# Kernel tuning notes

Measured on AMD Instinct MI355X. Metric: run time of the kernel, lower is better.

## Reference

```python
import jax, jax.numpy as jnp
import numpy as np

NC = 80          # num classes (len(yolov8.names))
CONF = 0.25      # ultralytics conf_thres default
IOU_T = 0.45     # ultralytics iou_thres default
MAX_DET = 300    # module default max_det
K = 1024         # pre-NMS candidate cap (static stand-in for max_nms)
MAX_WH = 7680.0  # ultralytics class-offset for multi-class NMS


def setup_inputs() -> dict:
    key = jax.random.key(0)
    k1, k2, k3 = jax.random.split(key, 3)
    B, A = 32, 8400
    # YOLOv8 head layout: rows 0:4 = xywh (pixels), rows 4: = sigmoid class scores
    xy = jax.random.uniform(k1, (B, 2, A), dtype=jnp.float32) * 640.0
    wh = jax.random.uniform(k2, (B, 2, A), dtype=jnp.float32) * 160.0 + 8.0
    scores = jax.random.uniform(k3, (B, NC, A), dtype=jnp.float32) ** 3  # mostly below conf_thres
    preds = jnp.concatenate([xy, wh, scores], axis=1)  # [B, 4+NC, A]
    return {"preds": preds}


def _box_iou(b):
    # b: [K, 4] xyxy -> [K, K] pairwise IoU
    area = (b[:, 2] - b[:, 0]) * (b[:, 3] - b[:, 1])
    lt = jnp.maximum(b[:, None, :2], b[None, :, :2])
    rb = jnp.minimum(b[:, None, 2:], b[None, :, 2:])
    wh = jnp.clip(rb - lt, 0.0)
    inter = wh[..., 0] * wh[..., 1]
    return inter / (area[:, None] + area[None, :] - inter + 1e-7)


def _nms_single(pred):
    # pred: [4+NC, A]
    boxes_xywh = pred[:4].T           # [A, 4]
    cls_scores = pred[4:].T           # [A, NC]
    conf = cls_scores.max(-1)         # best-class confidence per anchor
    cls = jnp.argmax(cls_scores, -1)
    score = jnp.where(conf > CONF, conf, 0.0)
    top, idx = jax.lax.top_k(score, K)            # K candidates by confidence
    xywh = boxes_xywh[idx]
    half = xywh[:, 2:] * 0.5
    boxes = jnp.concatenate([xywh[:, :2] - half, xywh[:, :2] + half], -1)  # xyxy
    cls_k = cls[idx]
    valid = top > CONF
    # multi-class NMS via per-class coordinate offset (ultralytics trick)
    iou = _box_iou(boxes + (cls_k.astype(boxes.dtype) * MAX_WH)[:, None])
    ar = jnp.arange(K)

    def body(i, st):
        supp, keep = st
        ki = valid[i] & ~supp[i]
        keep = keep.at[i].set(ki)
        supp = supp | (ki & (iou[i] > IOU_T) & (ar > i))
        return supp, keep

    _, keep = jax.lax.fori_loop(0, K, body,
                                (jnp.zeros(K, bool), jnp.zeros(K, bool)))
    fscore = jnp.where(keep, top, 0.0)
    sc, order = jax.lax.top_k(fscore, MAX_DET)
    det = jnp.concatenate(
        [boxes[order], top[order][:, None], cls_k[order].astype(boxes.dtype)[:, None]], -1)
    # pad invalid rows with value NC in every column (matches F.pad(value=len(names)))
    return jnp.where((sc > CONF)[:, None], det, jnp.float32(NC))


def reference(preds):
    # [B, MAX_DET, 6] -> (x1, y1, x2, y2, conf, cls), padded rows filled with NC
    return jax.vmap(_nms_single)(preds)
```

## Files before the change

### kernel.cpp

```cpp
#include <hip/hip_runtime.h>
#include <stdint.h>

typedef unsigned long long u64;
typedef unsigned int u32;

#define NC 80
#define CONF_T 0.25f
#define IOU_THR 0.45f
#define MAX_DET 300
#define KBIG 1024
#define A_ANCH 8400
#define NROWS 84
#define MAX_WH 7680.0f
#define HBINS 256
#define BIN_BASE 0x3e80u

__device__ __forceinline__ void hadd(u32* h, u32 bin, bool m, int lane) {
    u64 act = __ballot(m);
    if (act == 0) return;
    int fl = __ffsll((unsigned long long)act) - 1;
    u32 fb = __shfl(bin, fl);
    u64 same = __ballot(m && (bin == fb));
    if (lane == fl) atomicAdd(&h[fb], (u32)__popcll(same));
    if (m && (bin != fb)) atomicAdd(&h[bin], 1u);
}

__global__ __launch_bounds__(512) void yolo_conf_kernel(const float* __restrict__ preds,
                                                        u64* __restrict__ keys,
                                                        u32* __restrict__ hist) {
    int b = blockIdx.x / 9;
    int slab = blockIdx.x % 9;
    if (slab == 0 && threadIdx.x < HBINS) hist[(size_t)b * HBINS + threadIdx.x] = 0;
    int g = slab * 512 + threadIdx.x;
    if (g >= A_ANCH / 2) return;
    int a0 = g * 2;
    const float* base = preds + ((size_t)b * NROWS + 4) * A_ANCH + a0;
    float2 best = *(const float2*)base;
    int bc0 = 0, bc1 = 0;
#pragma unroll 8
    for (int c = 1; c < NC; ++c) {
        float2 v = *(const float2*)(base + (size_t)c * A_ANCH);
        if (v.x > best.x) { best.x = v.x; bc0 = c; }
        if (v.y > best.y) { best.y = v.y; bc1 = c; }
    }
    float s0 = (best.x > CONF_T) ? best.x : 0.0f;
    float s1 = (best.y > CONF_T) ? best.y : 0.0f;
    ulonglong2 kk;
    kk.x = ((u64)__float_as_uint(s0) << 32) | ((u64)(16383 - a0) << 7) | (u64)bc0;
    kk.y = ((u64)__float_as_uint(s1) << 32) | ((u64)(16383 - (a0 + 1)) << 7) | (u64)bc1;
    *(ulonglong2*)(keys + (size_t)b * A_ANCH + a0) = kk;
}

__global__ __launch_bounds__(256) void yolo_prep_kernel(const float* __restrict__ preds,
                                                        const u64* __restrict__ keys,
                                                        float4* __restrict__ obox,
                                                        u32* __restrict__ hist) {
    __shared__ u32 lh[HBINS];
    const int lane = threadIdx.x & 63;
    int b = blockIdx.x / 33;
    int a = (blockIdx.x % 33) * 256 + threadIdx.x;
    lh[threadIdx.x] = 0;
    __syncthreads();
    u32 bits = 0, bin = 0;
    bool act = a < A_ANCH;
    if (act) {
        u64 key = keys[(size_t)b * A_ANCH + a];
        bits = (u32)(key >> 32);
        int cls = (int)(key & 127u);
        const float* pb = preds + (size_t)b * NROWS * A_ANCH + a;
        float x = pb[0];
        float y = pb[A_ANCH];
        float w = pb[2 * A_ANCH];
        float h = pb[3 * A_ANCH];
        float hw = __fmul_rn(w, 0.5f), hh = __fmul_rn(h, 0.5f);
        float x1 = __fsub_rn(x, hw), x2 = __fadd_rn(x, hw);
        float y1 = __fsub_rn(y, hh), y2 = __fadd_rn(y, hh);
        float off = __fmul_rn((float)cls, MAX_WH);
        float4 oB;
        oB.x = __fadd_rn(x1, off); oB.y = __fadd_rn(y1, off);
        oB.z = __fadd_rn(x2, off); oB.w = __fadd_rn(y2, off);
        obox[(size_t)b * A_ANCH + a] = oB;
        bin = (bits >> 16) - BIN_BASE;
        if (bin > 255u) bin = 255u;
    }
    hadd(lh, bin, act && (bits != 0u), lane);
    __syncthreads();
    u32 c = lh[threadIdx.x];
    if (c) atomicAdd(&hist[(size_t)b * HBINS + threadIdx.x], c);
}

__device__ __forceinline__ float iou_f(float ix1, float iy1, float ix2, float iy2, float iar,
                                       float jx1, float jy1, float jx2, float jy2, float jar) {
    float lx = fmaxf(ix1, jx1), ly = fmaxf(iy1, jy1);
    float rx = fminf(ix2, jx2), ry = fminf(iy2, jy2);
    float ww = fmaxf(__fsub_rn(rx, lx), 0.0f);
    float hh = fmaxf(__fsub_rn(ry, ly), 0.0f);
    float inter = __fmul_rn(ww, hh);
    float den = __fadd_rn(__fsub_rn(__fadd_rn(iar, jar), inter), 1e-7f);
    return __fdiv_rn(inter, den);
}

__device__ __forceinline__ u64 bstep(u64 v, u32 idx, u32 size, u32 stride) {
    u64 v2 = __shfl_xor((unsigned long long)v, (int)stride, 64);
    bool keep_big = (((idx & stride) == 0) == ((idx & size) == 0));
    return ((v > v2) == keep_big) ? v : v2;
}

__device__ __forceinline__ void radix_scan(u32* hist, int nb, int shift, u32* s_scal,
                                           u32* wsum, int tid, int lane, int wid) {
    int per = nb >> 9; if (per == 0) per = 1;
    int na = nb / per;
    u32 rem = s_scal[1];
    u32 Pk = s_scal[0];
    int hi = nb - 1 - per * tid;
    u32 s = 0;
    if (tid < na)
        for (int q = 0; q < per; ++q) s += hist[hi - q];
    u32 pre = s;
#pragma unroll
    for (int off = 1; off < 64; off <<= 1) {
        u32 o = __shfl_up(pre, off);
        if (lane >= off) pre += o;
    }
    if (lane == 63) wsum[wid] = pre;
    __syncthreads();
    u32 base = 0;
    for (int w = 0; w < wid; ++w) base += wsum[w];
    u32 run = base + pre - s;
    if (tid < na) {
        for (int q = 0; q < per; ++q) {
            int d = hi - q;
            u32 g = hist[d];
            if (run < rem && rem <= run + g) {
                s_scal[0] = Pk | ((u32)d << shift);
                s_scal[1] = rem - run;
            }
            run += g;
        }
    }
    __syncthreads();
}

__global__ __launch_bounds__(512) void yolo_selsort_kernel(const u64* __restrict__ keys,
                                                           const u32* __restrict__ hist,
                                                           u64* __restrict__ sortk,
                                                           u32* __restrict__ meta) {
    const int b = blockIdx.x;
    const int tid = threadIdx.x;
    const int lane = tid & 63;
    const int wid = tid >> 6;

    __shared__ u64 skey[KBIG];
    __shared__ u32 wsum[8];
    __shared__ u32 s_scal[4];
    __shared__ u32 s_cnt;

    const u64* kb = keys + (size_t)b * A_ANCH;
    const u32* hb = hist + (size_t)b * HBINS;

    u32 hg = (tid < HBINS) ? hb[HBINS - 1 - tid] : 0u;
    u32 vals[17];
#pragma unroll
    for (int it = 0; it < 17; ++it) {
        int a = tid + it * 512;
        vals[it] = (a < A_ANCH) ? (u32)(kb[a] >> 32) : 0u;
    }
    {
        u32 pre = hg;
#pragma unroll
        for (int off = 1; off < 64; off <<= 1) {
            u32 o = __shfl_up(pre, off);
            if (lane >= off) pre += o;
        }
        if (lane == 63) wsum[wid] = pre;
        __syncthreads();
        u32 base = 0;
        for (int w = 0; w < wid; ++w) base += wsum[w];
        pre += base;
        u32 run = pre - hg;
        if (tid < HBINS) {
            if (run < 512u && 512u <= pre) { s_scal[0] = (u32)(HBINS - 1 - tid); s_scal[2] = pre; }
            if (tid == HBINS - 1) {
                s_scal[3] = pre;
                if (pre < 512u) { s_scal[0] = 0; s_scal[2] = pre; }
            }
        }
        __syncthreads();
    }
    const u32 Pbin16 = BIN_BASE + s_scal[0];
    const u32 Cfast = s_scal[2];
    const u32 validN = s_scal[3];
    if (tid == 0) { meta[b * 2] = Cfast; meta[b * 2 + 1] = validN; }
    if (Cfast > (u32)KBIG) return;

    skey[tid] = 0; skey[tid + 512] = 0;
    if (tid == 0) s_cnt = 0;
    __syncthreads();
#pragma unroll
    for (int it = 0; it < 17; ++it) {
        int a = tid + it * 512;
        u32 v = vals[it];
        bool take = (a < A_ANCH) && (v != 0u) && ((v >> 16) >= Pbin16);
        u64 m = __ballot(take);
        if (m) {
            int fl = __ffsll((unsigned long long)m) - 1;
            u32 basep = 0;
            if (lane == fl) basep = atomicAdd(&s_cnt, (u32)__popcll(m));
            basep = __shfl(basep, fl);
            if (take) {
                u32 pos = basep + (u32)__popcll(m & ((1ull << lane) - 1ull));
                if (pos < (u32)KBIG) skey[pos] = kb[a];
            }
        }
    }
    __syncthreads();

    {
        u64 vA = skey[tid], vB = skey[tid + 512];
        const u32 iA = (u32)tid, iB = (u32)tid + 512;
#pragma unroll
        for (u32 size = 2; size <= 64; size <<= 1)
#pragma unroll
            for (u32 stride = size >> 1; stride >= 1; stride >>= 1) {
                vA = bstep(vA, iA, size, stride);
                vB = bstep(vB, iB, size, stride);
            }
        skey[tid] = vA; skey[tid + 512] = vB;
        __syncthreads();
        for (u32 size = 128; size <= 1024; size <<= 1) {
            for (u32 stride = size >> 1; stride >= 64; stride >>= 1) {
                u32 i1 = ((tid & ~(int)(stride - 1)) << 1) | (tid & (stride - 1));
                u32 i2 = i1 + stride;
                bool desc = ((i1 & size) == 0);
                u64 x = skey[i1], y = skey[i2];
                if ((x < y) == desc) { skey[i1] = y; skey[i2] = x; }
                __syncthreads();
            }
            vA = skey[tid]; vB = skey[tid + 512];
#pragma unroll
            for (u32 stride = 32; stride >= 1; stride >>= 1) {
                vA = bstep(vA, iA, size, stride);
                vB = bstep(vB, iB, size, stride);
            }
            skey[tid] = vA; skey[tid + 512] = vB;
            __syncthreads();
        }
    }
    u64* so = sortk + (size_t)b * KBIG;
    so[tid] = skey[tid];
    so[tid + 512] = skey[tid + 512];
}

__global__ __launch_bounds__(512) void yolo_mat_kernel(const u64* __restrict__ sortk,
                                                       const float4* __restrict__ obox,
                                                       u64* __restrict__ rows) {
    const int b = blockIdx.x >> 3;
    const int m = blockIdx.x & 7;
    const int tid = threadIdx.x;
    const int lane = tid & 63;
    const int wid = tid >> 6;
    __shared__ float bx1[512], by1[512], bx2[512], by2[512], bar[512];

    const u64* sk = sortk + (size_t)b * KBIG;
    {
        u64 key = sk[tid];
        int idx = 16383 - (int)((key >> 7) & 16383u);
        if (idx >= A_ANCH || idx < 0) idx = 0;
        float4 ob = obox[(size_t)b * A_ANCH + idx];
        bx1[tid] = ob.x; by1[tid] = ob.y; bx2[tid] = ob.z; by2[tid] = ob.w;
        bar[tid] = __fmul_rn(__fsub_rn(ob.z, ob.x), __fsub_rn(ob.w, ob.y));
    }
    __syncthreads();

#pragma unroll
    for (int rr = 0; rr < 8; ++rr) {
        int i = m * 64 + wid * 8 + rr;
        float ix1 = bx1[i], iy1 = by1[i], ix2 = bx2[i], iy2 = by2[i], iar = bar[i];
        u64* rowp = rows + ((size_t)b * 512 + i) * 8;
#pragma unroll
        for (int wd = 0; wd < 8; ++wd) {
            int j = wd * 64 + lane;
            float iou = iou_f(ix1, iy1, ix2, iy2, iar, bx1[j], by1[j], bx2[j], by2[j], bar[j]);
            u64 mbit = __ballot((j > i) && (iou > IOU_THR));
            if (lane == 0) rowp[wd] = mbit;
        }
    }
}

union U2 {
    u32 hist[4096];
    struct { u32 eqw[264]; u32 wpre[264]; } tie;
};

__global__ __launch_bounds__(512) void yolo_recfb_kernel(const float* __restrict__ preds,
                                                         const u64* __restrict__ keys,
                                                         const u64* __restrict__ sortk,
                                                         const u64* __restrict__ rowsg,
                                                         const float4* __restrict__ obox,
                                                         const u32* __restrict__ hist,
                                                         const u32* __restrict__ meta,
                                                         float* __restrict__ out) {
    const int b = blockIdx.x;
    const int tid = threadIdx.x;
    const int lane = tid & 63;
    const int wid = tid >> 6;

    union SH {
        struct {
            u64 skl[512];
            u64 supp[8];
            u64 keep;
            int keptlist[364];
        } r;
        struct {
            U2 u2;
            u64 skey[KBIG];
            float BX1[KBIG], BY1[KBIG], BX2[KBIG], BY2[KBIG], BAR[KBIG];
            int keptlist[364];
            float kx1[364], ky1[364], kx2[364], ky2[364], kar[364];
            u32 kcls[364];
            u64 rows64[64];
        } f;
    };
    __shared__ SH sh;
    __shared__ u32 s_scal[4];
    __shared__ u32 wsum[8];
    __shared__ u32 s_cnt;
    __shared__ u32 s_csupp[2];
    __shared__ u32 s_nkept;

    const u32 Cfast0 = meta[b * 2];
    const u32 validN0 = meta[b * 2 + 1];

    sh.r.skl[tid] = sortk[(size_t)b * KBIG + tid];
    if (tid < 8) sh.r.supp[tid] = 0;
    if (tid == 0) s_nkept = 0;
    __syncthreads();

    bool ok = (Cfast0 <= (u32)KBIG);
    if (ok) {
        const u64* rb = rowsg + (size_t)b * 512 * 8;
        for (int c = 0; c < 8; ++c) {
            if (wid == 0) {
                int i = c * 64 + lane;
                u64 key = sh.r.skl[i];
                float sc = __uint_as_float((u32)(key >> 32));
                u64 ri = rb[(size_t)i * 8 + c];
                u64 validm = __ballot(sc > CONF_T) & ~sh.r.supp[c];
                u32 rlo = (u32)ri, rhi = (u32)(ri >> 32);
                u64 sup = 0, keep = 0;
#pragma unroll
                for (int i2 = 0; i2 < 64; ++i2) {
                    u64 rr = (((u64)(u32)__builtin_amdgcn_readlane((int)rhi, i2)) << 32) |
                             (u64)(u32)__builtin_amdgcn_readlane((int)rlo, i2);
                    bool ki = (((validm & ~sup) >> i2) & 1ull) != 0;
                    if (ki) { keep |= (1ull << i2); sup |= rr; }
                }
                u32 basek = s_nkept;
                if ((keep >> lane) & 1ull) {
                    u32 slot = basek + (u32)__popcll(keep & ((1ull << lane) - 1ull));
                    sh.r.keptlist[slot] = i;
                }
                if (lane == 0) { sh.r.keep = keep; s_nkept = basek + (u32)__popcll(keep); }
            }
            __syncthreads();
            {
                u64 k = sh.r.keep;
                u64 t = ((k >> lane) & 1ull) ? rb[(size_t)(c * 64 + lane) * 8 + wid] : 0ull;
#pragma unroll
                for (int off = 32; off >= 1; off >>= 1)
                    t |= (u64)__shfl_xor((unsigned long long)t, off, 64);
                if (lane == 0) sh.r.supp[wid] |= t;
            }
            __syncthreads();
            if (s_nkept >= MAX_DET) break;
        }
    }
    u32 nk0 = ok ? s_nkept : 0;
    bool fin = ok && ((nk0 >= MAX_DET) || (validN0 <= 512u));

    if (fin) {
        if (tid < MAX_DET) {
            float row[6];
            int t = (tid < (int)(nk0 < MAX_DET ? nk0 : MAX_DET)) ? sh.r.keptlist[tid] : -1;
            if (t >= 0) {
                u64 key = sh.r.skl[t];
                float score = __uint_as_float((u32)(key >> 32));
                int cls = (int)(key & 127u);
                int idx = 16383 - (int)((key >> 7) & 16383u);
                if (idx >= A_ANCH || idx < 0) idx = 0;
                const float* pb = preds + (size_t)b * NROWS * A_ANCH + idx;
                float x = pb[0], y = pb[A_ANCH], w = pb[2 * A_ANCH], h = pb[3 * A_ANCH];
                float hw = __fmul_rn(w, 0.5f), hh = __fmul_rn(h, 0.5f);
                row[0] = __fsub_rn(x, hw);
                row[1] = __fsub_rn(y, hh);
                row[2] = __fadd_rn(x, hw);
                row[3] = __fadd_rn(y, hh);
                row[4] = score;
                row[5] = (float)cls;
            } else {
                row[0] = row[1] = row[2] = row[3] = row[4] = row[5] = (float)NC;
            }
            float* o = out + ((size_t)b * MAX_DET + tid) * 6;
#pragma unroll
            for (int q = 0; q < 6; ++q) o[q] = row[q];
        }
        return;
    }

    __syncthreads();
    U2* u2 = &sh.f.u2;
    u64* skey = sh.f.skey;
    float* BX1 = sh.f.BX1; float* BY1 = sh.f.BY1;
    float* BX2 = sh.f.BX2; float* BY2 = sh.f.BY2; float* BAR = sh.f.BAR;
    int* keptlist = sh.f.keptlist;
    float* kx1 = sh.f.kx1; float* ky1 = sh.f.ky1;
    float* kx2 = sh.f.kx2; float* ky2 = sh.f.ky2; float* kar = sh.f.kar;
    u32* kcls = sh.f.kcls;
    u64* rows = sh.f.rows64;

    const u64* kb = keys + (size_t)b * A_ANCH;
    const u32* hb = hist + (size_t)b * HBINS;
    u32 hg = (tid < HBINS) ? hb[HBINS - 1 - tid] : 0u;
    u32 vals[17];
#pragma unroll
    for (int it = 0; it < 17; ++it) {
        int a = tid + it * 512;
        vals[it] = (a < A_ANCH) ? (u32)(kb[a] >> 32) : 0u;
    }
    {
        u32 pre = hg;
#pragma unroll
        for (int off = 1; off < 64; off <<= 1) {
            u32 o = __shfl_up(pre, off);
            if (lane >= off) pre += o;
        }
        if (lane == 63) wsum[wid] = pre;
        __syncthreads();
        u32 base = 0;
        for (int w = 0; w < wid; ++w) base += wsum[w];
        pre += base;
        u32 run = pre - hg;
        if (tid < HBINS) {
            if (run < 512u && 512u <= pre) { s_scal[0] = (u32)(HBINS - 1 - tid); s_scal[2] = pre; }
            if (tid == HBINS - 1) {
                s_scal[3] = pre;
                if (pre < 512u) { s_scal[0] = 0; s_scal[2] = pre; }
            }
        }
        __syncthreads();
    }
    const u32 Pbin16 = BIN_BASE + s_scal[0];
    const u32 Cfast = s_scal[2];
    const u32 validN = s_scal[3];

    for (int pass = 0; pass < 2; ++pass) {
        u32 Ccand;
        if (pass == 0) {
            if (Cfast > (u32)KBIG) continue;
            Ccand = Cfast;
            skey[tid] = 0; skey[tid + 512] = 0;
            if (tid == 0) { s_cnt = 0; s_nkept = 0; s_csupp[0] = 0; s_csupp[1] = 0; }
            __syncthreads();
#pragma unroll
            for (int it = 0; it < 17; ++it) {
                int a = tid + it * 512;
                u32 v = vals[it];
                bool take = (a < A_ANCH) && (v != 0u) && ((v >> 16) >= Pbin16);
                u64 m = __ballot(take);
                if (m) {
                    int fl = __ffsll((unsigned long long)m) - 1;
                    u32 basep = 0;
                    if (lane == fl) basep = atomicAdd(&s_cnt, (u32)__popcll(m));
                    basep = __shfl(basep, fl);
                    if (take) {
                        u32 pos = basep + (u32)__popcll(m & ((1ull << lane) - 1ull));
                        if (pos < (u32)KBIG) skey[pos] = kb[a];
                    }
                }
            }
            __syncthreads();
        } else {
            for (int i = tid; i < 4096; i += 512) u2->hist[i] = 0;
            if (tid == 0) {
                s_scal[0] = 0; s_scal[1] = (u32)KBIG; s_scal[2] = 0;
                s_nkept = 0; s_csupp[0] = 0; s_csupp[1] = 0;
            }
            __syncthreads();
#pragma unroll
            for (int it = 0; it < 17; ++it) {
                int a = tid + it * 512;
                hadd(u2->hist, vals[it] >> 20, a < A_ANCH, lane);
            }
            __syncthreads();
            radix_scan(u2->hist, 4096, 20, s_scal, wsum, tid, lane, wid);
            for (int i = tid; i < 4096; i += 512) u2->hist[i] = 0;
            __syncthreads();
            u32 Pk = s_scal[0];
#pragma unroll
            for (int it = 0; it < 17; ++it) {
                int a = tid + it * 512;
                u32 v = vals[it];
                bool m = (a < A_ANCH) && ((v & 0xFFF00000u) == Pk);
                hadd(u2->hist, (v >> 8) & 4095u, m, lane);
            }
            __syncthreads();
            radix_scan(u2->hist, 4096, 8, s_scal, wsum, tid, lane, wid);
            for (int i = tid; i < 256; i += 512) u2->hist[i] = 0;
            __syncthreads();
            Pk = s_scal[0];
#pragma unroll
            for (int it = 0; it < 17; ++it) {
                int a = tid + it * 512;
                u32 v = vals[it];
                bool m = (a < A_ANCH) && ((v & 0xFFFFFF00u) == Pk);
                hadd(u2->hist, v & 255u, m, lane);
            }
            __syncthreads();
            radix_scan(u2->hist, 256, 0, s_scal, wsum, tid, lane, wid);
            const u32 P = s_scal[0];
            const u32 tEq = s_scal[1];
            if (tid < 264) u2->tie.eqw[tid] = 0;
            __syncthreads();
#pragma unroll
            for (int it = 0; it < 17; ++it) {
                int a = tid + it * 512;
                if (a < A_ANCH && vals[it] == P) atomicOr(&u2->tie.eqw[a >> 5], 1u << (a & 31));
            }
            __syncthreads();
            if (wid == 0) {
                u32 cw[5], loc = 0;
#pragma unroll
                for (int q = 0; q < 5; ++q) {
                    int w2 = lane * 5 + q;
                    u32 e = (w2 < 264) ? u2->tie.eqw[w2] : 0u;
                    cw[q] = (u32)__popc(e); loc += cw[q];
                }
                u32 pre = loc;
#pragma unroll
                for (int off = 1; off < 64; off <<= 1) {
                    u32 o = __shfl_up(pre, off);
                    if (lane >= off) pre += o;
                }
                u32 run = pre - loc;
#pragma unroll
                for (int q = 0; q < 5; ++q) {
                    int w2 = lane * 5 + q;
                    if (w2 < 264) u2->tie.wpre[w2] = run;
                    run += cw[q];
                }
            }
            __syncthreads();
#pragma unroll
            for (int it = 0; it < 17; ++it) {
                int a = tid + it * 512;
                bool take = false;
                if (a < A_ANCH) {
                    u32 v = vals[it];
                    take = v > P;
                    if (!take && v == P) {
                        u32 r = u2->tie.wpre[a >> 5] +
                                (u32)__popc(u2->tie.eqw[a >> 5] & ((1u << (a & 31)) - 1u));
                        take = (r < tEq);
                    }
                }
                u64 m = __ballot(take);
                if (m) {
                    int fl = __ffsll((unsigned long long)m) - 1;
                    u32 basep = 0;
                    if (lane == fl) basep = atomicAdd(&s_scal[2], (u32)__popcll(m));
                    basep = __shfl(basep, fl);
                    if (take) {
                        u32 pos = basep + (u32)__popcll(m & ((1ull << lane) - 1ull));
                        if (pos < (u32)KBIG) skey[pos] = kb[a];
                    }
                }
            }
            __syncthreads();
            Ccand = KBIG;
        }

        {
            u64 vA = skey[tid], vB = skey[tid + 512];
            const u32 iA = (u32)tid, iB = (u32)tid + 512;
#pragma unroll
            for (u32 size = 2; size <= 64; size <<= 1)
#pragma unroll
                for (u32 stride = size >> 1; stride >= 1; stride >>= 1) {
                    vA = bstep(vA, iA, size, stride);
                    vB = bstep(vB, iB, size, stride);
                }
            skey[tid] = vA; skey[tid + 512] = vB;
            __syncthreads();
            for (u32 size = 128; size <= 1024; size <<= 1) {
                for (u32 stride = size >> 1; stride >= 64; stride >>= 1) {
                    u32 i1 = ((tid & ~(int)(stride - 1)) << 1) | (tid & (stride - 1));
                    u32 i2 = i1 + stride;
                    bool desc = ((i1 & size) == 0);
                    u64 x = skey[i1], y = skey[i2];
                    if ((x < y) == desc) { skey[i1] = y; skey[i2] = x; }
                    __syncthreads();
                }
                vA = skey[tid]; vB = skey[tid + 512];
#pragma unroll
                for (u32 stride = 32; stride >= 1; stride >>= 1) {
                    vA = bstep(vA, iA, size, stride);
                    vB = bstep(vB, iB, size, stride);
                }
                skey[tid] = vA; skey[tid + 512] = vB;
                __syncthreads();
            }
        }

#pragma unroll
        for (int q = 0; q < 2; ++q) {
            int t = tid + q * 512;
            u64 key = skey[t];
            int idx = 16383 - (int)((key >> 7) & 16383u);
            if (idx >= A_ANCH || idx < 0) idx = 0;
            float4 ob = obox[(size_t)b * A_ANCH + idx];
            BX1[t] = ob.x; BY1[t] = ob.y; BX2[t] = ob.z; BY2[t] = ob.w;
            BAR[t] = __fmul_rn(__fsub_rn(ob.z, ob.x), __fsub_rn(ob.w, ob.y));
        }
        __syncthreads();

        const int nchunks = (int)((Ccand + 63u) >> 6);
        for (int c = 0; c < nchunks; ++c) {
            int j = c * 64 + lane;
            u64 keyj = skey[j];
            float scj = __uint_as_float((u32)(keyj >> 32));
            u32 clsj = (u32)(keyj & 127u);
            float jx1 = BX1[j], jy1 = BY1[j], jx2 = BX2[j], jy2 = BY2[j], jar = BAR[j];

            u32 nk = s_nkept;
            bool suppbit = false;
            for (u32 k = wid; k < nk; k += 8) {
                bool cm = (kcls[k] == clsj);
                if (__ballot(cm)) {
                    float iou = iou_f(kx1[k], ky1[k], kx2[k], ky2[k], kar[k],
                                      jx1, jy1, jx2, jy2, jar);
                    suppbit |= (cm && (iou > IOU_THR));
                }
            }
            u64 bm = __ballot(suppbit);
            if (bm && lane == 0) {
                atomicOr(&s_csupp[0], (u32)bm);
                atomicOr(&s_csupp[1], (u32)(bm >> 32));
            }
#pragma unroll
            for (int p2 = 0; p2 < 8; ++p2) {
                int i = p2 * 8 + wid;
                int ci = c * 64 + i;
                u32 clsi = (u32)(skey[ci] & 127u);
                u64 m = 0;
                if (__ballot(clsi == clsj)) {
                    float iou = iou_f(BX1[ci], BY1[ci], BX2[ci], BY2[ci], BAR[ci],
                                      jx1, jy1, jx2, jy2, jar);
                    m = __ballot((lane > i) && (iou > IOU_THR));
                }
                if (lane == 0) rows[i] = m;
            }
            __syncthreads();
            if (wid == 0) {
                u64 row = rows[lane];
                u32 rlo = (u32)row, rhi = (u32)(row >> 32);
                u64 csupp = (((u64)s_csupp[1]) << 32) | (u64)s_csupp[0];
                u64 validm = __ballot(scj > CONF_T) & ~csupp;
                u64 supp = 0, keep = 0;
#pragma unroll
                for (int i = 0; i < 64; ++i) {
                    u64 ri = (((u64)(u32)__builtin_amdgcn_readlane((int)rhi, i)) << 32) |
                             (u64)(u32)__builtin_amdgcn_readlane((int)rlo, i);
                    bool ki = (((validm & ~supp) >> i) & 1ull) != 0;
                    if (ki) { keep |= (1ull << i); supp |= ri; }
                }
                u32 basek = s_nkept;
                if ((keep >> lane) & 1ull) {
                    u32 slot = basek + (u32)__popcll(keep & ((1ull << lane) - 1ull));
                    keptlist[slot] = j;
                    kx1[slot] = jx1; ky1[slot] = jy1;
                    kx2[slot] = jx2; ky2[slot] = jy2;
                    kar[slot] = jar; kcls[slot] = clsj;
                }
                if (lane == 0) {
                    s_nkept = basek + (u32)__popcll(keep);
                    s_csupp[0] = 0; s_csupp[1] = 0;
                }
            }
            __syncthreads();
            if (s_nkept >= MAX_DET) break;
        }

        u32 nk = s_nkept;
        bool finished = (nk >= MAX_DET) || (Ccand >= validN) || (pass == 1);
        if (!finished) continue;

        if (tid < MAX_DET) {
            float row[6];
            int t = (tid < (int)(nk < MAX_DET ? nk : MAX_DET)) ? keptlist[tid] : -1;
            if (t >= 0) {
                u64 key = skey[t];
                float score = __uint_as_float((u32)(key >> 32));
                int cls = (int)(key & 127u);
                int idx = 16383 - (int)((key >> 7) & 16383u);
                if (idx >= A_ANCH || idx < 0) idx = 0;
                const float* pb = preds + (size_t)b * NROWS * A_ANCH + idx;
                float x = pb[0], y = pb[A_ANCH], w = pb[2 * A_ANCH], h = pb[3 * A_ANCH];
                float hw = __fmul_rn(w, 0.5f), hh = __fmul_rn(h, 0.5f);
                row[0] = __fsub_rn(x, hw);
                row[1] = __fsub_rn(y, hh);
                row[2] = __fadd_rn(x, hw);
                row[3] = __fadd_rn(y, hh);
                row[4] = score;
                row[5] = (float)cls;
            } else {
                row[0] = row[1] = row[2] = row[3] = row[4] = row[5] = (float)NC;
            }
            float* o = out + ((size_t)b * MAX_DET + tid) * 6;
#pragma unroll
            for (int q = 0; q < 6; ++q) o[q] = row[q];
        }
        break;
    }
}

extern "C" void kernel_launch(void* const* d_in, const int* in_sizes, int n_in,
                              void* d_out, int out_size, void* d_ws, size_t ws_size,
                              hipStream_t stream) {
    const float* preds = (const float*)d_in[0];
    float* out = (float*)d_out;
    int B = in_sizes[0] / (NROWS * A_ANCH);
    float4* obox = (float4*)d_ws;
    u64* keys = (u64*)(obox + (size_t)B * A_ANCH);
    u64* sortk = keys + (size_t)B * A_ANCH;
    u64* rows = sortk + (size_t)B * KBIG;
    u32* hist = (u32*)(rows + (size_t)B * 512 * 8);
    u32* meta = hist + (size_t)B * HBINS;
    yolo_conf_kernel<<<dim3(B * 9), dim3(512), 0, stream>>>(preds, keys, hist);
    yolo_prep_kernel<<<dim3(B * 33), dim3(256), 0, stream>>>(preds, keys, obox, hist);
    yolo_selsort_kernel<<<dim3(B), dim3(512), 0, stream>>>(keys, hist, sortk, meta);
    yolo_mat_kernel<<<dim3(B * 8), dim3(512), 0, stream>>>(sortk, obox, rows);
    yolo_recfb_kernel<<<dim3(B), dim3(512), 0, stream>>>(preds, keys, sortk, rows, obox, hist, meta, out);
}
```

Before: 64.49 us.

## Fuse selection sort, IoU mask build and NMS reduction into one kernel

Merges the selsort, IoU-matrix and reduction kernels into a single per-image kernel. Sorted keys and the 512x8 suppression bitmask now stay in shared memory instead of round-tripping through global workspace, which removes two launches and the global traffic between them. In exchange, the IoU matrix is built by one 512-thread block per image instead of 8 blocks per image, so that phase gets less parallelism. The larger shared-memory footprint (about 56KB for the union) may also reduce occupancy.

```diff
diff --git a/kernel.cpp b/kernel.cpp
--- a/kernel.cpp
+++ b/kernel.cpp
@@ -141,164 +141,15 @@
     __syncthreads();
 }
 
-__global__ __launch_bounds__(512) void yolo_selsort_kernel(const u64* __restrict__ keys,
-                                                           const u32* __restrict__ hist,
-                                                           u64* __restrict__ sortk,
-                                                           u32* __restrict__ meta) {
-    const int b = blockIdx.x;
-    const int tid = threadIdx.x;
-    const int lane = tid & 63;
-    const int wid = tid >> 6;
-
-    __shared__ u64 skey[KBIG];
-    __shared__ u32 wsum[8];
-    __shared__ u32 s_scal[4];
-    __shared__ u32 s_cnt;
-
-    const u64* kb = keys + (size_t)b * A_ANCH;
-    const u32* hb = hist + (size_t)b * HBINS;
-
-    u32 hg = (tid < HBINS) ? hb[HBINS - 1 - tid] : 0u;
-    u32 vals[17];
-#pragma unroll
-    for (int it = 0; it < 17; ++it) {
-        int a = tid + it * 512;
-        vals[it] = (a < A_ANCH) ? (u32)(kb[a] >> 32) : 0u;
-    }
-    {
-        u32 pre = hg;
-#pragma unroll
-        for (int off = 1; off < 64; off <<= 1) {
-            u32 o = __shfl_up(pre, off);
-            if (lane >= off) pre += o;
-        }
-        if (lane == 63) wsum[wid] = pre;
-        __syncthreads();
-        u32 base = 0;
-        for (int w = 0; w < wid; ++w) base += wsum[w];
-        pre += base;
-        u32 run = pre - hg;
-        if (tid < HBINS) {
-            if (run < 512u && 512u <= pre) { s_scal[0] = (u32)(HBINS - 1 - tid); s_scal[2] = pre; }
-            if (tid == HBINS - 1) {
-                s_scal[3] = pre;
-                if (pre < 512u) { s_scal[0] = 0; s_scal[2] = pre; }
-            }
-        }
-        __syncthreads();
-    }
-    const u32 Pbin16 = BIN_BASE + s_scal[0];
-    const u32 Cfast = s_scal[2];
-    const u32 validN = s_scal[3];
-    if (tid == 0) { meta[b * 2] = Cfast; meta[b * 2 + 1] = validN; }
-    if (Cfast > (u32)KBIG) return;
-
-    skey[tid] = 0; skey[tid + 512] = 0;
-    if (tid == 0) s_cnt = 0;
-    __syncthreads();
-#pragma unroll
-    for (int it = 0; it < 17; ++it) {
-        int a = tid + it * 512;
-        u32 v = vals[it];
-        bool take = (a < A_ANCH) && (v != 0u) && ((v >> 16) >= Pbin16);
-        u64 m = __ballot(take);
-        if (m) {
-            int fl = __ffsll((unsigned long long)m) - 1;
-            u32 basep = 0;
-            if (lane == fl) basep = atomicAdd(&s_cnt, (u32)__popcll(m));
-            basep = __shfl(basep, fl);
-            if (take) {
-                u32 pos = basep + (u32)__popcll(m & ((1ull << lane) - 1ull));
-                if (pos < (u32)KBIG) skey[pos] = kb[a];
-            }
-        }
-    }
-    __syncthreads();
-
-    {
-        u64 vA = skey[tid], vB = skey[tid + 512];
-        const u32 iA = (u32)tid, iB = (u32)tid + 512;
-#pragma unroll
-        for (u32 size = 2; size <= 64; size <<= 1)
-#pragma unroll
-            for (u32 stride = size >> 1; stride >= 1; stride >>= 1) {
-                vA = bstep(vA, iA, size, stride);
-                vB = bstep(vB, iB, size, stride);
-            }
-        skey[tid] = vA; skey[tid + 512] = vB;
-        __syncthreads();
-        for (u32 size = 128; size <= 1024; size <<= 1) {
-            for (u32 stride = size >> 1; stride >= 64; stride >>= 1) {
-                u32 i1 = ((tid & ~(int)(stride - 1)) << 1) | (tid & (stride - 1));
-                u32 i2 = i1 + stride;
-                bool desc = ((i1 & size) == 0);
-                u64 x = skey[i1], y = skey[i2];
-                if ((x < y) == desc) { skey[i1] = y; skey[i2] = x; }
-                __syncthreads();
-            }
-            vA = skey[tid]; vB = skey[tid + 512];
-#pragma unroll
-            for (u32 stride = 32; stride >= 1; stride >>= 1) {
-                vA = bstep(vA, iA, size, stride);
-                vB = bstep(vB, iB, size, stride);
-            }
-            skey[tid] = vA; skey[tid + 512] = vB;
-            __syncthreads();
-        }
-    }
-    u64* so = sortk + (size_t)b * KBIG;
-    so[tid] = skey[tid];
-    so[tid + 512] = skey[tid + 512];
-}
-
-__global__ __launch_bounds__(512) void yolo_mat_kernel(const u64* __restrict__ sortk,
-                                                       const float4* __restrict__ obox,
-                                                       u64* __restrict__ rows) {
-    const int b = blockIdx.x >> 3;
-    const int m = blockIdx.x & 7;
-    const int tid = threadIdx.x;
-    const int lane = tid & 63;
-    const int wid = tid >> 6;
-    __shared__ float bx1[512], by1[512], bx2[512], by2[512], bar[512];
-
-    const u64* sk = sortk + (size_t)b * KBIG;
-    {
-        u64 key = sk[tid];
-        int idx = 16383 - (int)((key >> 7) & 16383u);
-        if (idx >= A_ANCH || idx < 0) idx = 0;
-        float4 ob = obox[(size_t)b * A_ANCH + idx];
-        bx1[tid] = ob.x; by1[tid] = ob.y; bx2[tid] = ob.z; by2[tid] = ob.w;
-        bar[tid] = __fmul_rn(__fsub_rn(ob.z, ob.x), __fsub_rn(ob.w, ob.y));
-    }
-    __syncthreads();
-
-#pragma unroll
-    for (int rr = 0; rr < 8; ++rr) {
-        int i = m * 64 + wid * 8 + rr;
-        float ix1 = bx1[i], iy1 = by1[i], ix2 = bx2[i], iy2 = by2[i], iar = bar[i];
-        u64* rowp = rows + ((size_t)b * 512 + i) * 8;
-#pragma unroll
-        for (int wd = 0; wd < 8; ++wd) {
-            int j = wd * 64 + lane;
-            float iou = iou_f(ix1, iy1, ix2, iy2, iar, bx1[j], by1[j], bx2[j], by2[j], bar[j]);
-            u64 mbit = __ballot((j > i) && (iou > IOU_THR));
-            if (lane == 0) rowp[wd] = mbit;
-        }
-    }
-}
-
 union U2 {
     u32 hist[4096];
     struct { u32 eqw[264]; u32 wpre[264]; } tie;
 };
 
-__global__ __launch_bounds__(512) void yolo_recfb_kernel(const float* __restrict__ preds,
+__global__ __launch_bounds__(512) void yolo_fused_kernel(const float* __restrict__ preds,
                                                          const u64* __restrict__ keys,
-                                                         const u64* __restrict__ sortk,
-                                                         const u64* __restrict__ rowsg,
                                                          const float4* __restrict__ obox,
                                                          const u32* __restrict__ hist,
-                                                         const u32* __restrict__ meta,
                                                          float* __restrict__ out) {
     const int b = blockIdx.x;
     const int tid = threadIdx.x;
@@ -307,10 +158,12 @@
 
     union SH {
         struct {
-            u64 skl[512];
+            u64 skey[KBIG];
+            float BX1[512], BY1[512], BX2[512], BY2[512], BAR[512];
+            u64 rowsL[512 * 8];
+            int keptlist[364];
             u64 supp[8];
             u64 keep;
-            int keptlist[364];
         } r;
         struct {
             U2 u2;
@@ -329,23 +182,138 @@
     __shared__ u32 s_csupp[2];
     __shared__ u32 s_nkept;
 
-    const u32 Cfast0 = meta[b * 2];
-    const u32 validN0 = meta[b * 2 + 1];
-
-    sh.r.skl[tid] = sortk[(size_t)b * KBIG + tid];
-    if (tid < 8) sh.r.supp[tid] = 0;
-    if (tid == 0) s_nkept = 0;
-    __syncthreads();
-
-    bool ok = (Cfast0 <= (u32)KBIG);
+    const u64* kb = keys + (size_t)b * A_ANCH;
+    const u32* hb = hist + (size_t)b * HBINS;
+
+    u32 hg = (tid < HBINS) ? hb[HBINS - 1 - tid] : 0u;
+    u32 vals[17];
+#pragma unroll
+    for (int it = 0; it < 17; ++it) {
+        int a = tid + it * 512;
+        vals[it] = (a < A_ANCH) ? (u32)(kb[a] >> 32) : 0u;
+    }
+    {
+        u32 pre = hg;
+#pragma unroll
+        for (int off = 1; off < 64; off <<= 1) {
+            u32 o = __shfl_up(pre, off);
+            if (lane >= off) pre += o;
+        }
+        if (lane == 63) wsum[wid] = pre;
+        __syncthreads();
+        u32 base = 0;
+        for (int w = 0; w < wid; ++w) base += wsum[w];
+        pre += base;
+        u32 run = pre - hg;
+        if (tid < HBINS) {
+            if (run < 512u && 512u <= pre) { s_scal[0] = (u32)(HBINS - 1 - tid); s_scal[2] = pre; }
+            if (tid == HBINS - 1) {
+                s_scal[3] = pre;
+                if (pre < 512u) { s_scal[0] = 0; s_scal[2] = pre; }
+            }
+        }
+        __syncthreads();
+    }
+    const u32 Pbin16 = BIN_BASE + s_scal[0];
+    const u32 Cfast = s_scal[2];
+    const u32 validN = s_scal[3];
+
+    bool ok = (Cfast <= (u32)KBIG);
+    u32 nk0 = 0;
+
     if (ok) {
-        const u64* rb = rowsg + (size_t)b * 512 * 8;
+        sh.r.skey[tid] = 0; sh.r.skey[tid + 512] = 0;
+        if (tid == 0) s_cnt = 0;
+        __syncthreads();
+#pragma unroll
+        for (int it = 0; it < 17; ++it) {
+            int a = tid + it * 512;
+            u32 v = vals[it];
+            bool take = (a < A_ANCH) && (v != 0u) && ((v >> 16) >= Pbin16);
+            u64 m = __ballot(take);
+            if (m) {
+                int fl = __ffsll((unsigned long long)m) - 1;
+                u32 basep = 0;
+                if (lane == fl) basep = atomicAdd(&s_cnt, (u32)__popcll(m));
+                basep = __shfl(basep, fl);
+                if (take) {
+                    u32 pos = basep + (u32)__popcll(m & ((1ull << lane) - 1ull));
+                    if (pos < (u32)KBIG) sh.r.skey[pos] = kb[a];
+                }
+            }
+        }
+        __syncthreads();
+
+        {
+            u64 vA = sh.r.skey[tid], vB = sh.r.skey[tid + 512];
+            const u32 iA = (u32)tid, iB = (u32)tid + 512;
+#pragma unroll
+            for (u32 size = 2; size <= 64; size <<= 1)
+#pragma unroll
+                for (u32 stride = size >> 1; stride >= 1; stride >>= 1) {
+                    vA = bstep(vA, iA, size, stride);
+                    vB = bstep(vB, iB, size, stride);
+                }
+            sh.r.skey[tid] = vA; sh.r.skey[tid + 512] = vB;
+            __syncthreads();
+            for (u32 size = 128; size <= 1024; size <<= 1) {
+                for (u32 stride = size >> 1; stride >= 64; stride >>= 1) {
+                    u32 i1 = ((tid & ~(int)(stride - 1)) << 1) | (tid & (stride - 1));
+                    u32 i2 = i1 + stride;
+                    bool desc = ((i1 & size) == 0);
+                    u64 x = sh.r.skey[i1], y = sh.r.skey[i2];
+                    if ((x < y) == desc) { sh.r.skey[i1] = y; sh.r.skey[i2] = x; }
+                    __syncthreads();
+                }
+                vA = sh.r.skey[tid]; vB = sh.r.skey[tid + 512];
+#pragma unroll
+                for (u32 stride = 32; stride >= 1; stride >>= 1) {
+                    vA = bstep(vA, iA, size, stride);
+                    vB = bstep(vB, iB, size, stride);
+                }
+                sh.r.skey[tid] = vA; sh.r.skey[tid + 512] = vB;
+                __syncthreads();
+            }
+        }
+
+        {
+            u64 key = sh.r.skey[tid];
+            int idx = 16383 - (int)((key >> 7) & 16383u);
+            if (idx >= A_ANCH || idx < 0) idx = 0;
+            float4 ob = obox[(size_t)b * A_ANCH + idx];
+            sh.r.BX1[tid] = ob.x; sh.r.BY1[tid] = ob.y;
+            sh.r.BX2[tid] = ob.z; sh.r.BY2[tid] = ob.w;
+            sh.r.BAR[tid] = __fmul_rn(__fsub_rn(ob.z, ob.x), __fsub_rn(ob.w, ob.y));
+        }
+        if (tid < 8) sh.r.supp[tid] = 0;
+        if (tid == 0) s_nkept = 0;
+        __syncthreads();
+
+#pragma unroll
+        for (int m = 0; m < 8; ++m) {
+#pragma unroll
+            for (int rr = 0; rr < 8; ++rr) {
+                int i = m * 64 + wid * 8 + rr;
+                float ix1 = sh.r.BX1[i], iy1 = sh.r.BY1[i];
+                float ix2 = sh.r.BX2[i], iy2 = sh.r.BY2[i], iar = sh.r.BAR[i];
+#pragma unroll
+                for (int wd = 0; wd < 8; ++wd) {
+                    int j = wd * 64 + lane;
+                    float iou = iou_f(ix1, iy1, ix2, iy2, iar,
+                                      sh.r.BX1[j], sh.r.BY1[j], sh.r.BX2[j], sh.r.BY2[j], sh.r.BAR[j]);
+                    u64 mbit = __ballot((j > i) && (iou > IOU_THR));
+                    if (lane == 0) sh.r.rowsL[i * 8 + wd] = mbit;
+                }
+            }
+        }
+        __syncthreads();
+
         for (int c = 0; c < 8; ++c) {
             if (wid == 0) {
                 int i = c * 64 + lane;
-                u64 key = sh.r.skl[i];
+                u64 key = sh.r.skey[i];
                 float sc = __uint_as_float((u32)(key >> 32));
-                u64 ri = rb[(size_t)i * 8 + c];
+                u64 ri = sh.r.rowsL[i * 8 + c];
                 u64 validm = __ballot(sc > CONF_T) & ~sh.r.supp[c];
                 u32 rlo = (u32)ri, rhi = (u32)(ri >> 32);
                 u64 sup = 0, keep = 0;
@@ -366,7 +334,7 @@
             __syncthreads();
             {
                 u64 k = sh.r.keep;
-                u64 t = ((k >> lane) & 1ull) ? rb[(size_t)(c * 64 + lane) * 8 + wid] : 0ull;
+                u64 t = ((k >> lane) & 1ull) ? sh.r.rowsL[(c * 64 + lane) * 8 + wid] : 0ull;
 #pragma unroll
                 for (int off = 32; off >= 1; off >>= 1)
                     t |= (u64)__shfl_xor((unsigned long long)t, off, 64);
@@ -375,16 +343,16 @@
             __syncthreads();
             if (s_nkept >= MAX_DET) break;
         }
-    }
-    u32 nk0 = ok ? s_nkept : 0;
-    bool fin = ok && ((nk0 >= MAX_DET) || (validN0 <= 512u));
+        nk0 = s_nkept;
+    }
+    bool fin = ok && ((nk0 >= MAX_DET) || (validN <= 512u));
 
     if (fin) {
         if (tid < MAX_DET) {
             float row[6];
             int t = (tid < (int)(nk0 < MAX_DET ? nk0 : MAX_DET)) ? sh.r.keptlist[tid] : -1;
             if (t >= 0) {
-                u64 key = sh.r.skl[t];
+                u64 key = sh.r.skey[t];
                 float score = __uint_as_float((u32)(key >> 32));
                 int cls = (int)(key & 127u);
                 int idx = 16383 - (int)((key >> 7) & 16383u);
@@ -418,41 +386,6 @@
     float* kx2 = sh.f.kx2; float* ky2 = sh.f.ky2; float* kar = sh.f.kar;
     u32* kcls = sh.f.kcls;
     u64* rows = sh.f.rows64;
-
-    const u64* kb = keys + (size_t)b * A_ANCH;
-    const u32* hb = hist + (size_t)b * HBINS;
-    u32 hg = (tid < HBINS) ? hb[HBINS - 1 - tid] : 0u;
-    u32 vals[17];
-#pragma unroll
-    for (int it = 0; it < 17; ++it) {
-        int a = tid + it * 512;
-        vals[it] = (a < A_ANCH) ? (u32)(kb[a] >> 32) : 0u;
-    }
-    {
-        u32 pre = hg;
-#pragma unroll
-        for (int off = 1; off < 64; off <<= 1) {
-            u32 o = __shfl_up(pre, off);
-            if (lane >= off) pre += o;
-        }
-        if (lane == 63) wsum[wid] = pre;
-        __syncthreads();
-        u32 base = 0;
-        for (int w = 0; w < wid; ++w) base += wsum[w];
-        pre += base;
-        u32 run = pre - hg;
-        if (tid < HBINS) {
-            if (run < 512u && 512u <= pre) { s_scal[0] = (u32)(HBINS - 1 - tid); s_scal[2] = pre; }
-            if (tid == HBINS - 1) {
-                s_scal[3] = pre;
-                if (pre < 512u) { s_scal[0] = 0; s_scal[2] = pre; }
-            }
-        }
-        __syncthreads();
-    }
-    const u32 Pbin16 = BIN_BASE + s_scal[0];
-    const u32 Cfast = s_scal[2];
-    const u32 validN = s_scal[3];
 
     for (int pass = 0; pass < 2; ++pass) {
         u32 Ccand;
@@ -732,13 +665,8 @@
     int B = in_sizes[0] / (NROWS * A_ANCH);
     float4* obox = (float4*)d_ws;
     u64* keys = (u64*)(obox + (size_t)B * A_ANCH);
-    u64* sortk = keys + (size_t)B * A_ANCH;
-    u64* rows = sortk + (size_t)B * KBIG;
-    u32* hist = (u32*)(rows + (size_t)B * 512 * 8);
-    u32* meta = hist + (size_t)B * HBINS;
+    u32* hist = (u32*)(keys + (size_t)B * A_ANCH);
     yolo_conf_kernel<<<dim3(B * 9), dim3(512), 0, stream>>>(preds, keys, hist);
     yolo_prep_kernel<<<dim3(B * 33), dim3(256), 0, stream>>>(preds, keys, obox, hist);
-    yolo_selsort_kernel<<<dim3(B), dim3(512), 0, stream>>>(keys, hist, sortk, meta);
-    yolo_mat_kernel<<<dim3(B * 8), dim3(512), 0, stream>>>(sortk, obox, rows);
-    yolo_recfb_kernel<<<dim3(B), dim3(512), 0, stream>>>(preds, keys, sortk, rows, obox, hist, meta, out);
-}
+    yolo_fused_kernel<<<dim3(B), dim3(512), 0, stream>>>(preds, keys, obox, hist, out);
+}
```

After: 97.86 us. +51.7%, slower.
